# Optimization experiments

Measured on AMD Instinct MI355X. Metric: run time of the kernel, lower is better.

The kernel has to match this reference:

```python
import jax, jax.numpy as jnp
import numpy as np


def setup_inputs() -> dict:
    key = jax.random.key(0)
    k1, k2, k3 = jax.random.split(key, 3)
    N, D, C, G = 200000, 256, 512, 512
    x = jax.random.normal(k1, (N, D), dtype=jnp.float32)
    centroid_weight = jax.random.normal(k2, (C, D), dtype=jnp.float32)
    graph = jnp.sort(jax.random.randint(k3, (N,), 0, G, dtype=jnp.int64))
    return {"x": x, "centroid_weight": centroid_weight, "graph": graph, "num_graphs": G}


def reference(x, centroid_weight, graph, num_graphs):
    # EuclideanManifold: exp map at origin is the identity; dist is the L2 norm.
    # Pairwise node-to-centroid L2 distances via the GEMM identity
    # ||a-b||^2 = ||a||^2 + ||b||^2 - 2 a.b  (same math as the expanded
    # unsqueeze/expand path, without materializing the [N, C, D] tensor).
    x_sq = jnp.sum(x * x, axis=-1, keepdims=True)              # [N, 1]
    c_sq = jnp.sum(centroid_weight * centroid_weight, axis=-1)  # [C]
    sq = x_sq + c_sq[None, :] - 2.0 * jnp.einsum("nd,cd->nc", x, centroid_weight)
    dist = jnp.sqrt(jnp.maximum(sq, 0.0))                       # [N, C]

    # AvgPooling: per-graph mean of node-to-centroid distances.
    sums = jax.ops.segment_sum(dist, graph, num_segments=num_graphs)           # [G, C]
    counts = jax.ops.segment_sum(jnp.ones((dist.shape[0],), dist.dtype), graph,
                                 num_segments=num_graphs)                      # [G]
    return sums / jnp.maximum(counts, 1.0)[:, None]
```

## Files before the change

### kernel.cpp

```cpp
#include <hip/hip_runtime.h>
#include <hip/hip_bf16.h>

typedef __attribute__((ext_vector_type(8))) short short8;
typedef __attribute__((ext_vector_type(4))) float f32x4;
typedef __attribute__((ext_vector_type(2))) unsigned int uint2v;
typedef __attribute__((ext_vector_type(4))) unsigned int uint4v;

#define DK 256
#define BM 128
#define BN 128
#define BK 64
#define NKT 4

__device__ __forceinline__ unsigned int pack2bf(float lo, float hi) {
  return __builtin_amdgcn_perm(__builtin_bit_cast(unsigned int, hi),
                               __builtin_bit_cast(unsigned int, lo), 0x07060302);
}

__device__ __forceinline__ uint4v make_srsrc(const void* p, unsigned bytes) {
  union { const void* p; unsigned u[2]; } a; a.p = p;
  uint4v r;
  r.x = a.u[0];
  r.y = a.u[1] & 0xFFFFu;
  r.z = bytes;
  r.w = 0x00020000u;
  return r;
}

__global__ void __launch_bounds__(256)
prep_w(const float* __restrict__ w, unsigned short* __restrict__ wbf,
       float* __restrict__ csq) {
  const int b = blockIdx.x;
  const int ct = b >> 2, kt = b & 3;
  const int t = threadIdx.x;
  const int col = t >> 1, khalf = t & 1;
  const float* src = w + (size_t)(ct * BN + col) * DK + kt * BK + khalf * 32;
  unsigned char* dst = (unsigned char*)wbf + (size_t)b * 16384;
  const int sw = (col & 7) << 4;
  float s = 0.f;
  #pragma unroll
  for (int jc = 0; jc < 4; ++jc) {
    f32x4 v0 = *reinterpret_cast<const f32x4*>(src + jc * 8);
    f32x4 v1 = *reinterpret_cast<const f32x4*>(src + jc * 8 + 4);
    s += v0.x*v0.x + v0.y*v0.y + v0.z*v0.z + v0.w*v0.w
       + v1.x*v1.x + v1.y*v1.y + v1.z*v1.z + v1.w*v1.w;
    uint4v pk = { pack2bf(v0.x,v0.y), pack2bf(v0.z,v0.w),
                  pack2bf(v1.x,v1.y), pack2bf(v1.z,v1.w) };
    const int cidx = khalf * 4 + jc;
    *reinterpret_cast<uint4v*>(dst + ((col * 128 + cidx * 16) ^ sw)) = pk;
  }
  s += __shfl_xor(s, 1);
  if (khalf == 0) atomicAdd(&csq[ct * BN + col], s);
}

template<bool PREW>
__global__ void __launch_bounds__(256, 2)
centroid_gemm_pool(const float* __restrict__ x, const float* __restrict__ w,
                   const unsigned short* __restrict__ wbf,
                   const float* __restrict__ csqg, const int* __restrict__ graph,
                   float* __restrict__ outsum, int* __restrict__ cnt,
                   int N, int C, int row_tiles)
{
  __shared__ __align__(16) unsigned char lds_a[16384];
  __shared__ __align__(16) unsigned char lds_b[2][16384];
  __shared__ float xsq_lds[BM];
  __shared__ float csq_lds[BN];

  const int bid = blockIdx.x;
  const int xcd = bid & 7;
  const int j   = bid >> 3;
  const int ct  = j & 3;
  const int rt  = (j >> 2) * 8 + xcd;
  if (rt >= row_tiles) return;

  const int t    = threadIdx.x;
  const int lane = t & 63;
  const int wid  = t >> 6;
  const int wr   = wid >> 1, wc = wid & 1;
  const int h    = lane >> 4, l15 = lane & 15;

  const int g16 = t >> 4;
  const int sc4 = t & 15;
  const uint4v xrsrc = make_srsrc(x, (unsigned)((size_t)N * DK * 4));
  const unsigned voffA = (unsigned)(rt * BM + g16) * (DK * 4) + sc4 * 16;

  const int awbase = (g16 * 128 + sc4 * 8) ^ ((g16 & 7) << 4);
  const int base_a = (wr * 8192 + l15 * 128 + h * 16) ^ ((l15 & 7) << 4);
  const int base_b = (wc * 8192 + l15 * 128 + h * 16) ^ ((l15 & 7) << 4);

  const int rowg = rt * BM + wr * 64 + lane;
  int gl = (rowg < N) ? graph[rowg] : -1;
  asm volatile("" : "+v"(gl));

  f32x4 acc[4][4];
  #pragma unroll
  for (int mt = 0; mt < 4; ++mt)
    #pragma unroll
    for (int nt = 0; nt < 4; ++nt)
      acc[mt][nt] = (f32x4){0.f, 0.f, 0.f, 0.f};
  f32x4 accx[4];
  #pragma unroll
  for (int mt = 0; mt < 4; ++mt) accx[mt] = (f32x4){0.f, 0.f, 0.f, 0.f};
  float cq[8] = {0.f,0.f,0.f,0.f,0.f,0.f,0.f,0.f};

  f32x4 ra[8];
  auto loadA = [&](int kt) {
    #pragma unroll
    for (int q = 0; q < 8; ++q)
      asm volatile("buffer_load_dwordx4 %0, %1, %2, %3 offen"
                   : "=v"(ra[q])
                   : "v"(voffA), "s"(xrsrc), "s"(q * 16 * DK * 4 + kt * BK * 4));
  };
  auto cvtA = [&]() {
    #pragma unroll
    for (int q = 0; q < 8; ++q) {
      f32x4 v = ra[q];
      uint2v pk = { pack2bf(v.x, v.y), pack2bf(v.z, v.w) };
      *reinterpret_cast<uint2v*>(lds_a + awbase + q * 2048) = pk;
    }
  };
  auto stageB = [&](int buf, int kt) {
    const unsigned short* src = wbf + (((size_t)ct * 4 + kt) << 13) + t * 8;
    unsigned char* dst = lds_b[buf] + t * 16;
    #pragma unroll
    for (int p = 0; p < 4; ++p)
      __builtin_amdgcn_global_load_lds(src + p * 2048, dst + p * 4096, 16, 0, 0);
  };
  auto stageBsync = [&](int buf, int kt, bool accum) {
    #pragma unroll
    for (int q = 0; q < 8; ++q) {
      const int colq = q * 16 + g16;
      f32x4 v = *reinterpret_cast<const f32x4*>(
          w + (size_t)(ct * BN + colq) * DK + kt * BK + sc4 * 4);
      if (accum) cq[q] += v.x*v.x + v.y*v.y + v.z*v.z + v.w*v.w;
      uint2v pk = { pack2bf(v.x, v.y), pack2bf(v.z, v.w) };
      *reinterpret_cast<uint2v*>(lds_b[buf] + awbase + q * 2048) = pk;
    }
  };
  auto compute = [&](unsigned char* lb) {
    __builtin_amdgcn_s_setprio(1);
    #pragma unroll
    for (int kk = 0; kk < 2; ++kk) {
      short8 af[4], bfr[4];
      const int ka = base_a ^ (kk << 6);
      const int kb = base_b ^ (kk << 6);
      #pragma unroll
      for (int mt = 0; mt < 4; ++mt)
        af[mt] = *reinterpret_cast<const short8*>(lds_a + ka + mt * 2048);
      #pragma unroll
      for (int nt = 0; nt < 4; ++nt)
        bfr[nt] = *reinterpret_cast<const short8*>(lb + kb + nt * 2048);
      #pragma unroll
      for (int mt = 0; mt < 4; ++mt)
        #pragma unroll
        for (int nt = 0; nt < 4; ++nt)
          acc[mt][nt] = __builtin_amdgcn_mfma_f32_16x16x32_bf16(af[mt], bfr[nt], acc[mt][nt], 0, 0, 0);
      if (wc == 0) {
        #pragma unroll
        for (int mt = 0; mt < 4; ++mt)
          accx[mt] = __builtin_amdgcn_mfma_f32_16x16x32_bf16(af[mt], af[mt], accx[mt], 0, 0, 0);
      }
    }
    __builtin_amdgcn_s_setprio(0);
  };

  loadA(0);
  if (PREW) stageB(0, 0); else stageBsync(0, 0, true);

  #pragma unroll
  for (int kt = 0; kt < NKT; ++kt) {
    const int cur = kt & 1;
    if (PREW) { asm volatile("s_waitcnt vmcnt(4)" ::: "memory"); }
    else      { asm volatile("s_waitcnt vmcnt(0)" ::: "memory"); }
    __builtin_amdgcn_sched_barrier(0);
    cvtA();
    if (kt + 1 < NKT) {
      loadA(kt + 1);
      if (PREW) stageB(cur ^ 1, kt + 1);
      else      stageBsync(cur ^ 1, kt + 1, kt == 0);
      if (PREW) { asm volatile("s_waitcnt vmcnt(12)" ::: "memory"); }
      else      { asm volatile("s_waitcnt vmcnt(0)" ::: "memory"); }
    } else {
      asm volatile("s_waitcnt vmcnt(0)" ::: "memory");
    }
    asm volatile("s_waitcnt lgkmcnt(0)" ::: "memory");
    __builtin_amdgcn_sched_barrier(0);
    __builtin_amdgcn_s_barrier();
    __builtin_amdgcn_sched_barrier(0);
    compute(lds_b[cur]);
    __builtin_amdgcn_sched_barrier(0);
    __builtin_amdgcn_s_barrier();
    __builtin_amdgcn_sched_barrier(0);
  }

  if (wc == 0 && h == (l15 >> 2)) {
    #pragma unroll
    for (int mt = 0; mt < 4; ++mt)
      xsq_lds[wr * 64 + mt * 16 + l15] = accx[mt][l15 & 3];
  }
  if (!PREW) {
    #pragma unroll
    for (int q = 0; q < 8; ++q) {
      float sb = cq[q];
      sb += __shfl_xor(sb, 1); sb += __shfl_xor(sb, 2);
      sb += __shfl_xor(sb, 4); sb += __shfl_xor(sb, 8);
      if (l15 == 0) csq_lds[q * 16 + g16] = sb;
    }
  }
  __syncthreads();

  float xs[4][4], cs[4];
  #pragma unroll
  for (int mt = 0; mt < 4; ++mt)
    #pragma unroll
    for (int i = 0; i < 4; ++i)
      xs[mt][i] = xsq_lds[wr * 64 + mt * 16 + h * 4 + i];
  #pragma unroll
  for (int nt = 0; nt < 4; ++nt)
    cs[nt] = PREW ? csqg[ct * BN + wc * 64 + nt * 16 + l15]
                  : csq_lds[wc * 64 + nt * 16 + l15];
  #pragma unroll
  for (int mt = 0; mt < 4; ++mt)
    #pragma unroll
    for (int nt = 0; nt < 4; ++nt)
      #pragma unroll
      for (int i = 0; i < 4; ++i) {
        float dd = fmaf(-2.0f, acc[mt][nt][i], xs[mt][i] + cs[nt]);
        acc[mt][nt][i] = __builtin_amdgcn_sqrtf(fmaxf(dd, 0.f));
      }

  const int col0 = ct * BN + wc * 64;
  const int glp  = __shfl_up(gl, 1);
  const unsigned long long bmw = __ballot(lane == 0 || gl != glp);

  int s0 = 0;
  while (s0 < 64) {
    unsigned long long rest = (s0 < 63) ? (bmw >> (s0 + 1)) : 0ULL;
    const int e = rest ? s0 + 1 + __builtin_ctzll(rest) : 64;
    const int g = __shfl(gl, s0);
    if (g >= 0) {
      float p[4] = {0.f, 0.f, 0.f, 0.f};
      #pragma unroll
      for (int mt = 0; mt < 4; ++mt)
        #pragma unroll
        for (int i = 0; i < 4; ++i) {
          const int row = mt * 16 + h * 4 + i;
          const bool in = (row >= s0) && (row < e);
          #pragma unroll
          for (int nt = 0; nt < 4; ++nt)
            p[nt] += in ? acc[mt][nt][i] : 0.f;
        }
      #pragma unroll
      for (int nt = 0; nt < 4; ++nt) {
        p[nt] += __shfl_xor(p[nt], 16);
        p[nt] += __shfl_xor(p[nt], 32);
      }
      if (lane < 16) {
        #pragma unroll
        for (int nt = 0; nt < 4; ++nt)
          atomicAdd(&outsum[(size_t)g * C + col0 + nt * 16 + lane], p[nt]);
      }
      if (cnt && ct == 0 && wc == 0 && lane == 0)
        atomicAdd(&cnt[g], e - s0);
    }
    s0 = e;
  }
}

__global__ void __launch_bounds__(256)
divide_counts(float* __restrict__ out, const int* __restrict__ cnt, int C)
{
  const int g = blockIdx.x;
  const int c0 = cnt[g];
  const float inv = 1.0f / (float)(c0 > 1 ? c0 : 1);
  for (int c = threadIdx.x; c < C; c += 256)
    out[(size_t)g * C + c] *= inv;
}

__global__ void __launch_bounds__(128)
divide_by_count(float* __restrict__ out, const int* __restrict__ graph, int N, int C)
{
  const int g = blockIdx.x;
  int lo = 0, hi = N;
  while (lo < hi) { int mid = (lo + hi) >> 1; if (graph[mid] < g) lo = mid + 1; else hi = mid; }
  const int lb = lo;
  hi = N;
  while (lo < hi) { int mid = (lo + hi) >> 1; if (graph[mid] <= g) lo = mid + 1; else hi = mid; }
  const int cntg = lo - lb;
  const float inv = 1.0f / (float)(cntg > 1 ? cntg : 1);
  for (int c = threadIdx.x; c < C; c += blockDim.x)
    out[(size_t)g * C + c] *= inv;
}

extern "C" void kernel_launch(void* const* d_in, const int* in_sizes, int n_in,
                              void* d_out, int out_size, void* d_ws, size_t ws_size,
                              hipStream_t stream) {
  const float* x     = (const float*)d_in[0];
  const float* w     = (const float*)d_in[1];
  const int*   graph = (const int*)d_in[2];
  const int N = in_sizes[2];
  const int D = in_sizes[0] / N;
  const int C = in_sizes[1] / D;
  const int G = out_size / C;

  const int row_tiles = (N + BM - 1) / BM;
  const int rgroups   = (row_tiles + 7) / 8;
  const int grid      = rgroups * 8 * (C / BN);

  const size_t wbf_bytes = (size_t)16 * 16384;
  const size_t csq_off   = wbf_bytes;
  const size_t cnt_off   = wbf_bytes + (size_t)C * 4;
  const bool prew     = ws_size >= cnt_off + (size_t)G * 4;
  const bool have_cnt = prew || ws_size >= (size_t)G * 4;

  unsigned short* wbf = (unsigned short*)d_ws;
  float* csq = (float*)((char*)d_ws + csq_off);
  int*   cnt = prew ? (int*)((char*)d_ws + cnt_off)
                    : (have_cnt ? (int*)d_ws : nullptr);

  hipMemsetAsync(d_out, 0, (size_t)out_size * sizeof(float), stream);
  if (cnt) hipMemsetAsync(cnt, 0, (size_t)G * sizeof(int), stream);

  if (prew) {
    hipMemsetAsync(csq, 0, (size_t)C * sizeof(float), stream);
    prep_w<<<dim3(16), dim3(256), 0, stream>>>(w, wbf, csq);
    centroid_gemm_pool<true><<<dim3(grid), dim3(256), 0, stream>>>(
        x, w, wbf, csq, graph, (float*)d_out, cnt, N, C, row_tiles);
  } else {
    centroid_gemm_pool<false><<<dim3(grid), dim3(256), 0, stream>>>(
        x, w, wbf, csq, graph, (float*)d_out, cnt, N, C, row_tiles);
  }

  if (cnt)
    divide_counts<<<dim3(G), dim3(256), 0, stream>>>((float*)d_out, cnt, C);
  else
    divide_by_count<<<dim3(G), dim3(128), 0, stream>>>((float*)d_out, graph, N, C);
}
```

Before: 98.76 us.

## Give each wave private A rows and overlap B staging with compute

```diff
diff --git a/kernel.cpp b/kernel.cpp
--- a/kernel.cpp
+++ b/kernel.cpp
@@ -76,31 +76,31 @@
   const int t    = threadIdx.x;
   const int lane = t & 63;
   const int wid  = t >> 6;
-  const int wr   = wid >> 1, wc = wid & 1;
   const int h    = lane >> 4, l15 = lane & 15;
+
+  const uint4v xrsrc = make_srsrc(x, (unsigned)((size_t)N * DK * 4));
+  const unsigned voffA = (unsigned)(rt * BM + wid * 32 + h) * (DK * 4) + l15 * 16;
+
+  const int base_a = wid * 4096 + ((l15 * 128 + h * 16) ^ ((l15 & 7) << 4));
+  const int base_b = (l15 * 128 + h * 16) ^ ((l15 & 7) << 4);
 
   const int g16 = t >> 4;
   const int sc4 = t & 15;
-  const uint4v xrsrc = make_srsrc(x, (unsigned)((size_t)N * DK * 4));
-  const unsigned voffA = (unsigned)(rt * BM + g16) * (DK * 4) + sc4 * 16;
-
-  const int awbase = (g16 * 128 + sc4 * 8) ^ ((g16 & 7) << 4);
-  const int base_a = (wr * 8192 + l15 * 128 + h * 16) ^ ((l15 & 7) << 4);
-  const int base_b = (wc * 8192 + l15 * 128 + h * 16) ^ ((l15 & 7) << 4);
-
-  const int rowg = rt * BM + wr * 64 + lane;
+  const int awbase_b = (g16 * 128 + sc4 * 8) ^ ((g16 & 7) << 4);
+
+  const int rowg = rt * BM + wid * 32 + (lane & 31);
   int gl = (rowg < N) ? graph[rowg] : -1;
   asm volatile("" : "+v"(gl));
 
-  f32x4 acc[4][4];
-  #pragma unroll
-  for (int mt = 0; mt < 4; ++mt)
-    #pragma unroll
-    for (int nt = 0; nt < 4; ++nt)
+  f32x4 acc[2][8];
+  #pragma unroll
+  for (int mt = 0; mt < 2; ++mt)
+    #pragma unroll
+    for (int nt = 0; nt < 8; ++nt)
       acc[mt][nt] = (f32x4){0.f, 0.f, 0.f, 0.f};
-  f32x4 accx[4];
-  #pragma unroll
-  for (int mt = 0; mt < 4; ++mt) accx[mt] = (f32x4){0.f, 0.f, 0.f, 0.f};
+  f32x4 accx[2];
+  accx[0] = (f32x4){0.f,0.f,0.f,0.f};
+  accx[1] = (f32x4){0.f,0.f,0.f,0.f};
   float cq[8] = {0.f,0.f,0.f,0.f,0.f,0.f,0.f,0.f};
 
   f32x4 ra[8];
@@ -109,14 +109,16 @@
     for (int q = 0; q < 8; ++q)
       asm volatile("buffer_load_dwordx4 %0, %1, %2, %3 offen"
                    : "=v"(ra[q])
-                   : "v"(voffA), "s"(xrsrc), "s"(q * 16 * DK * 4 + kt * BK * 4));
+                   : "v"(voffA), "s"(xrsrc), "s"(q * 4096 + kt * 256));
   };
   auto cvtA = [&]() {
     #pragma unroll
     for (int q = 0; q < 8; ++q) {
       f32x4 v = ra[q];
       uint2v pk = { pack2bf(v.x, v.y), pack2bf(v.z, v.w) };
-      *reinterpret_cast<uint2v*>(lds_a + awbase + q * 2048) = pk;
+      const int rl = q * 4 + h;
+      *reinterpret_cast<uint2v*>(lds_a + wid * 4096 +
+          ((rl * 128 + l15 * 8) ^ ((rl & 7) << 4))) = pk;
     }
   };
   auto stageB = [&](int buf, int kt) {
@@ -134,32 +136,25 @@
           w + (size_t)(ct * BN + colq) * DK + kt * BK + sc4 * 4);
       if (accum) cq[q] += v.x*v.x + v.y*v.y + v.z*v.z + v.w*v.w;
       uint2v pk = { pack2bf(v.x, v.y), pack2bf(v.z, v.w) };
-      *reinterpret_cast<uint2v*>(lds_b[buf] + awbase + q * 2048) = pk;
+      *reinterpret_cast<uint2v*>(lds_b[buf] + awbase_b + q * 2048) = pk;
     }
   };
   auto compute = [&](unsigned char* lb) {
     __builtin_amdgcn_s_setprio(1);
     #pragma unroll
     for (int kk = 0; kk < 2; ++kk) {
-      short8 af[4], bfr[4];
       const int ka = base_a ^ (kk << 6);
       const int kb = base_b ^ (kk << 6);
+      short8 af0 = *reinterpret_cast<const short8*>(lds_a + ka);
+      short8 af1 = *reinterpret_cast<const short8*>(lds_a + ka + 2048);
       #pragma unroll
-      for (int mt = 0; mt < 4; ++mt)
-        af[mt] = *reinterpret_cast<const short8*>(lds_a + ka + mt * 2048);
-      #pragma unroll
-      for (int nt = 0; nt < 4; ++nt)
-        bfr[nt] = *reinterpret_cast<const short8*>(lb + kb + nt * 2048);
-      #pragma unroll
-      for (int mt = 0; mt < 4; ++mt)
-        #pragma unroll
-        for (int nt = 0; nt < 4; ++nt)
-          acc[mt][nt] = __builtin_amdgcn_mfma_f32_16x16x32_bf16(af[mt], bfr[nt], acc[mt][nt], 0, 0, 0);
-      if (wc == 0) {
-        #pragma unroll
-        for (int mt = 0; mt < 4; ++mt)
-          accx[mt] = __builtin_amdgcn_mfma_f32_16x16x32_bf16(af[mt], af[mt], accx[mt], 0, 0, 0);
+      for (int nt = 0; nt < 8; ++nt) {
+        short8 bfr = *reinterpret_cast<const short8*>(lb + kb + nt * 2048);
+        acc[0][nt] = __builtin_amdgcn_mfma_f32_16x16x32_bf16(af0, bfr, acc[0][nt], 0, 0, 0);
+        acc[1][nt] = __builtin_amdgcn_mfma_f32_16x16x32_bf16(af1, bfr, acc[1][nt], 0, 0, 0);
       }
+      accx[0] = __builtin_amdgcn_mfma_f32_16x16x32_bf16(af0, af0, accx[0], 0, 0, 0);
+      accx[1] = __builtin_amdgcn_mfma_f32_16x16x32_bf16(af1, af1, accx[1], 0, 0, 0);
     }
     __builtin_amdgcn_s_setprio(0);
   };
@@ -176,9 +171,7 @@
     cvtA();
     if (kt + 1 < NKT) {
       loadA(kt + 1);
-      if (PREW) stageB(cur ^ 1, kt + 1);
-      else      stageBsync(cur ^ 1, kt + 1, kt == 0);
-      if (PREW) { asm volatile("s_waitcnt vmcnt(12)" ::: "memory"); }
+      if (PREW) { asm volatile("s_waitcnt vmcnt(8)" ::: "memory"); }
       else      { asm volatile("s_waitcnt vmcnt(0)" ::: "memory"); }
     } else {
       asm volatile("s_waitcnt vmcnt(0)" ::: "memory");
@@ -187,16 +180,16 @@
     __builtin_amdgcn_sched_barrier(0);
     __builtin_amdgcn_s_barrier();
     __builtin_amdgcn_sched_barrier(0);
+    if (kt + 1 < NKT) {
+      if (PREW) stageB(cur ^ 1, kt + 1);
+      else      stageBsync(cur ^ 1, kt + 1, kt == 0);
+    }
     compute(lds_b[cur]);
-    __builtin_amdgcn_sched_barrier(0);
-    __builtin_amdgcn_s_barrier();
-    __builtin_amdgcn_sched_barrier(0);
-  }
-
-  if (wc == 0 && h == (l15 >> 2)) {
-    #pragma unroll
-    for (int mt = 0; mt < 4; ++mt)
-      xsq_lds[wr * 64 + mt * 16 + l15] = accx[mt][l15 & 3];
+  }
+
+  if (h == (l15 >> 2)) {
+    xsq_lds[wid * 32 + l15]      = accx[0][l15 & 3];
+    xsq_lds[wid * 32 + 16 + l15] = accx[1][l15 & 3];
   }
   if (!PREW) {
     #pragma unroll
@@ -206,61 +199,61 @@
       sb += __shfl_xor(sb, 4); sb += __shfl_xor(sb, 8);
       if (l15 == 0) csq_lds[q * 16 + g16] = sb;
     }
-  }
-  __syncthreads();
-
-  float xs[4][4], cs[4];
-  #pragma unroll
-  for (int mt = 0; mt < 4; ++mt)
+    __syncthreads();
+  }
+
+  float xs[2][4], cs[8];
+  #pragma unroll
+  for (int mt = 0; mt < 2; ++mt)
     #pragma unroll
     for (int i = 0; i < 4; ++i)
-      xs[mt][i] = xsq_lds[wr * 64 + mt * 16 + h * 4 + i];
-  #pragma unroll
-  for (int nt = 0; nt < 4; ++nt)
-    cs[nt] = PREW ? csqg[ct * BN + wc * 64 + nt * 16 + l15]
-                  : csq_lds[wc * 64 + nt * 16 + l15];
-  #pragma unroll
-  for (int mt = 0; mt < 4; ++mt)
-    #pragma unroll
-    for (int nt = 0; nt < 4; ++nt)
+      xs[mt][i] = xsq_lds[wid * 32 + mt * 16 + h * 4 + i];
+  #pragma unroll
+  for (int nt = 0; nt < 8; ++nt)
+    cs[nt] = PREW ? csqg[ct * BN + nt * 16 + l15] : csq_lds[nt * 16 + l15];
+  #pragma unroll
+  for (int mt = 0; mt < 2; ++mt)
+    #pragma unroll
+    for (int nt = 0; nt < 8; ++nt)
       #pragma unroll
       for (int i = 0; i < 4; ++i) {
         float dd = fmaf(-2.0f, acc[mt][nt][i], xs[mt][i] + cs[nt]);
         acc[mt][nt][i] = __builtin_amdgcn_sqrtf(fmaxf(dd, 0.f));
       }
 
-  const int col0 = ct * BN + wc * 64;
+  const int col0 = ct * BN;
   const int glp  = __shfl_up(gl, 1);
-  const unsigned long long bmw = __ballot(lane == 0 || gl != glp);
+  const unsigned int m32 =
+      (unsigned int)(__ballot(lane == 0 || gl != glp) & 0xffffffffull);
 
   int s0 = 0;
-  while (s0 < 64) {
-    unsigned long long rest = (s0 < 63) ? (bmw >> (s0 + 1)) : 0ULL;
-    const int e = rest ? s0 + 1 + __builtin_ctzll(rest) : 64;
+  while (s0 < 32) {
+    unsigned int rest = (s0 < 31) ? (m32 >> (s0 + 1)) : 0u;
+    const int e = rest ? s0 + 1 + __builtin_ctz(rest) : 32;
     const int g = __shfl(gl, s0);
     if (g >= 0) {
-      float p[4] = {0.f, 0.f, 0.f, 0.f};
+      float p[8] = {0.f,0.f,0.f,0.f,0.f,0.f,0.f,0.f};
       #pragma unroll
-      for (int mt = 0; mt < 4; ++mt)
+      for (int mt = 0; mt < 2; ++mt)
         #pragma unroll
         for (int i = 0; i < 4; ++i) {
           const int row = mt * 16 + h * 4 + i;
           const bool in = (row >= s0) && (row < e);
           #pragma unroll
-          for (int nt = 0; nt < 4; ++nt)
+          for (int nt = 0; nt < 8; ++nt)
             p[nt] += in ? acc[mt][nt][i] : 0.f;
         }
       #pragma unroll
-      for (int nt = 0; nt < 4; ++nt) {
+      for (int nt = 0; nt < 8; ++nt) {
         p[nt] += __shfl_xor(p[nt], 16);
         p[nt] += __shfl_xor(p[nt], 32);
       }
       if (lane < 16) {
         #pragma unroll
-        for (int nt = 0; nt < 4; ++nt)
+        for (int nt = 0; nt < 8; ++nt)
           atomicAdd(&outsum[(size_t)g * C + col0 + nt * 16 + lane], p[nt]);
       }
-      if (cnt && ct == 0 && wc == 0 && lane == 0)
+      if (cnt && ct == 0 && lane == 0)
         atomicAdd(&cnt[g], e - s0);
     }
     s0 = e;
```

New measurement: 104.0 us. +5.3%, slower.

## Process two row tiles per block with cross-tile load prefetch

Applied to the files above, without the earlier changes.

```diff
diff --git a/kernel.cpp b/kernel.cpp
--- a/kernel.cpp
+++ b/kernel.cpp
@@ -70,8 +70,11 @@
   const int xcd = bid & 7;
   const int j   = bid >> 3;
   const int ct  = j & 3;
-  const int rt  = (j >> 2) * 8 + xcd;
-  if (rt >= row_tiles) return;
+  const int rp  = (j >> 2) * 8 + xcd;
+  const int n_pairs = (row_tiles + 1) >> 1;
+  if (rp >= n_pairs) return;
+  const int rt0 = rp * 2;
+  const bool two = (rt0 + 1 < row_tiles);
 
   const int t    = threadIdx.x;
   const int lane = t & 63;
@@ -82,15 +85,20 @@
   const int g16 = t >> 4;
   const int sc4 = t & 15;
   const uint4v xrsrc = make_srsrc(x, (unsigned)((size_t)N * DK * 4));
-  const unsigned voffA = (unsigned)(rt * BM + g16) * (DK * 4) + sc4 * 16;
+  const unsigned voffA0 = (unsigned)(rt0 * BM + g16) * (DK * 4) + sc4 * 16;
 
   const int awbase = (g16 * 128 + sc4 * 8) ^ ((g16 & 7) << 4);
   const int base_a = (wr * 8192 + l15 * 128 + h * 16) ^ ((l15 & 7) << 4);
   const int base_b = (wc * 8192 + l15 * 128 + h * 16) ^ ((l15 & 7) << 4);
 
-  const int rowg = rt * BM + wr * 64 + lane;
-  int gl = (rowg < N) ? graph[rowg] : -1;
-  asm volatile("" : "+v"(gl));
+  int gl0, gl1;
+  {
+    const int r0 = rt0 * BM + wr * 64 + lane;
+    gl0 = (r0 < N) ? graph[r0] : -1;
+    const int r1 = r0 + BM;
+    gl1 = (two && r1 < N) ? graph[r1] : -1;
+  }
+  asm volatile("" : "+v"(gl0), "+v"(gl1));
 
   f32x4 acc[4][4];
   #pragma unroll
@@ -104,12 +112,12 @@
   float cq[8] = {0.f,0.f,0.f,0.f,0.f,0.f,0.f,0.f};
 
   f32x4 ra[8];
-  auto loadA = [&](int kt) {
+  auto loadA = [&](unsigned vo, int kt) {
     #pragma unroll
     for (int q = 0; q < 8; ++q)
       asm volatile("buffer_load_dwordx4 %0, %1, %2, %3 offen"
                    : "=v"(ra[q])
-                   : "v"(voffA), "s"(xrsrc), "s"(q * 16 * DK * 4 + kt * BK * 4));
+                   : "v"(vo), "s"(xrsrc), "s"(q * 16 * DK * 4 + kt * BK * 4));
   };
   auto cvtA = [&]() {
     #pragma unroll
@@ -164,106 +172,134 @@
     __builtin_amdgcn_s_setprio(0);
   };
 
-  loadA(0);
+  loadA(voffA0, 0);
   if (PREW) stageB(0, 0); else stageBsync(0, 0, true);
 
   #pragma unroll
-  for (int kt = 0; kt < NKT; ++kt) {
-    const int cur = kt & 1;
-    if (PREW) { asm volatile("s_waitcnt vmcnt(4)" ::: "memory"); }
-    else      { asm volatile("s_waitcnt vmcnt(0)" ::: "memory"); }
-    __builtin_amdgcn_sched_barrier(0);
-    cvtA();
-    if (kt + 1 < NKT) {
-      loadA(kt + 1);
-      if (PREW) stageB(cur ^ 1, kt + 1);
-      else      stageBsync(cur ^ 1, kt + 1, kt == 0);
-      if (PREW) { asm volatile("s_waitcnt vmcnt(12)" ::: "memory"); }
-      else      { asm volatile("s_waitcnt vmcnt(0)" ::: "memory"); }
-    } else {
-      asm volatile("s_waitcnt vmcnt(0)" ::: "memory");
-    }
-    asm volatile("s_waitcnt lgkmcnt(0)" ::: "memory");
-    __builtin_amdgcn_sched_barrier(0);
-    __builtin_amdgcn_s_barrier();
-    __builtin_amdgcn_sched_barrier(0);
-    compute(lds_b[cur]);
-    __builtin_amdgcn_sched_barrier(0);
-    __builtin_amdgcn_s_barrier();
-    __builtin_amdgcn_sched_barrier(0);
-  }
-
-  if (wc == 0 && h == (l15 >> 2)) {
+  for (int r2 = 0; r2 < 2; ++r2) {
+    if (r2 == 1 && !two) break;
+    const int rt = rt0 + r2;
+    const unsigned vo = voffA0 + (unsigned)r2 * (BM * DK * 4);
+    #pragma unroll
+    for (int kt = 0; kt < NKT; ++kt) {
+      const int cur = kt & 1;
+      if (PREW) {
+        if (r2 == 1 && kt == 0) { asm volatile("s_waitcnt vmcnt(0)" ::: "memory"); }
+        else                    { asm volatile("s_waitcnt vmcnt(4)" ::: "memory"); }
+      } else {
+        asm volatile("s_waitcnt vmcnt(0)" ::: "memory");
+      }
+      __builtin_amdgcn_sched_barrier(0);
+      cvtA();
+      const bool last_global = (kt == NKT - 1) && (r2 == 1 || !two);
+      if (!last_global) {
+        if (kt + 1 < NKT) {
+          loadA(vo, kt + 1);
+          if (PREW) stageB(cur ^ 1, kt + 1);
+          else      stageBsync(cur ^ 1, kt + 1, r2 == 0 && kt == 0);
+        } else {
+          loadA(vo + BM * DK * 4, 0);
+          if (PREW) stageB(cur ^ 1, 0);
+          else      stageBsync(cur ^ 1, 0, false);
+        }
+        if (PREW) { asm volatile("s_waitcnt vmcnt(12)" ::: "memory"); }
+        else      { asm volatile("s_waitcnt vmcnt(0)" ::: "memory"); }
+      } else {
+        asm volatile("s_waitcnt vmcnt(0)" ::: "memory");
+      }
+      asm volatile("s_waitcnt lgkmcnt(0)" ::: "memory");
+      __builtin_amdgcn_sched_barrier(0);
+      __builtin_amdgcn_s_barrier();
+      __builtin_amdgcn_sched_barrier(0);
+      compute(lds_b[cur]);
+      __builtin_amdgcn_sched_barrier(0);
+      __builtin_amdgcn_s_barrier();
+      __builtin_amdgcn_sched_barrier(0);
+    }
+
+    if (wc == 0 && h == (l15 >> 2)) {
+      #pragma unroll
+      for (int mt = 0; mt < 4; ++mt)
+        xsq_lds[wr * 64 + mt * 16 + l15] = accx[mt][l15 & 3];
+    }
+    if (!PREW && r2 == 0) {
+      #pragma unroll
+      for (int q = 0; q < 8; ++q) {
+        float sb = cq[q];
+        sb += __shfl_xor(sb, 1); sb += __shfl_xor(sb, 2);
+        sb += __shfl_xor(sb, 4); sb += __shfl_xor(sb, 8);
+        if (l15 == 0) csq_lds[q * 16 + g16] = sb;
+      }
+    }
+    __syncthreads();
+
+    float xs[4][4], cs[4];
     #pragma unroll
     for (int mt = 0; mt < 4; ++mt)
-      xsq_lds[wr * 64 + mt * 16 + l15] = accx[mt][l15 & 3];
-  }
-  if (!PREW) {
-    #pragma unroll
-    for (int q = 0; q < 8; ++q) {
-      float sb = cq[q];
-      sb += __shfl_xor(sb, 1); sb += __shfl_xor(sb, 2);
-      sb += __shfl_xor(sb, 4); sb += __shfl_xor(sb, 8);
-      if (l15 == 0) csq_lds[q * 16 + g16] = sb;
-    }
-  }
-  __syncthreads();
-
-  float xs[4][4], cs[4];
-  #pragma unroll
-  for (int mt = 0; mt < 4; ++mt)
-    #pragma unroll
-    for (int i = 0; i < 4; ++i)
-      xs[mt][i] = xsq_lds[wr * 64 + mt * 16 + h * 4 + i];
-  #pragma unroll
-  for (int nt = 0; nt < 4; ++nt)
-    cs[nt] = PREW ? csqg[ct * BN + wc * 64 + nt * 16 + l15]
-                  : csq_lds[wc * 64 + nt * 16 + l15];
-  #pragma unroll
-  for (int mt = 0; mt < 4; ++mt)
+      #pragma unroll
+      for (int i = 0; i < 4; ++i)
+        xs[mt][i] = xsq_lds[wr * 64 + mt * 16 + h * 4 + i];
     #pragma unroll
     for (int nt = 0; nt < 4; ++nt)
-      #pragma unroll
-      for (int i = 0; i < 4; ++i) {
-        float dd = fmaf(-2.0f, acc[mt][nt][i], xs[mt][i] + cs[nt]);
-        acc[mt][nt][i] = __builtin_amdgcn_sqrtf(fmaxf(dd, 0.f));
-      }
-
-  const int col0 = ct * BN + wc * 64;
-  const int glp  = __shfl_up(gl, 1);
-  const unsigned long long bmw = __ballot(lane == 0 || gl != glp);
-
-  int s0 = 0;
-  while (s0 < 64) {
-    unsigned long long rest = (s0 < 63) ? (bmw >> (s0 + 1)) : 0ULL;
-    const int e = rest ? s0 + 1 + __builtin_ctzll(rest) : 64;
-    const int g = __shfl(gl, s0);
-    if (g >= 0) {
-      float p[4] = {0.f, 0.f, 0.f, 0.f};
-      #pragma unroll
-      for (int mt = 0; mt < 4; ++mt)
+      cs[nt] = PREW ? csqg[ct * BN + wc * 64 + nt * 16 + l15]
+                    : csq_lds[wc * 64 + nt * 16 + l15];
+    #pragma unroll
+    for (int mt = 0; mt < 4; ++mt)
+      #pragma unroll
+      for (int nt = 0; nt < 4; ++nt)
         #pragma unroll
         for (int i = 0; i < 4; ++i) {
-          const int row = mt * 16 + h * 4 + i;
-          const bool in = (row >= s0) && (row < e);
+          float dd = fmaf(-2.0f, acc[mt][nt][i], xs[mt][i] + cs[nt]);
+          acc[mt][nt][i] = __builtin_amdgcn_sqrtf(fmaxf(dd, 0.f));
+        }
+
+    const int col0 = ct * BN + wc * 64;
+    const int gl   = r2 ? gl1 : gl0;
+    const int glp  = __shfl_up(gl, 1);
+    const unsigned long long bmw = __ballot(lane == 0 || gl != glp);
+
+    int s0 = 0;
+    while (s0 < 64) {
+      unsigned long long rest = (s0 < 63) ? (bmw >> (s0 + 1)) : 0ULL;
+      const int e = rest ? s0 + 1 + __builtin_ctzll(rest) : 64;
+      const int g = __shfl(gl, s0);
+      if (g >= 0) {
+        float p[4] = {0.f, 0.f, 0.f, 0.f};
+        #pragma unroll
+        for (int mt = 0; mt < 4; ++mt)
+          #pragma unroll
+          for (int i = 0; i < 4; ++i) {
+            const int row = mt * 16 + h * 4 + i;
+            const bool in = (row >= s0) && (row < e);
+            #pragma unroll
+            for (int nt = 0; nt < 4; ++nt)
+              p[nt] += in ? acc[mt][nt][i] : 0.f;
+          }
+        #pragma unroll
+        for (int nt = 0; nt < 4; ++nt) {
+          p[nt] += __shfl_xor(p[nt], 16);
+          p[nt] += __shfl_xor(p[nt], 32);
+        }
+        if (lane < 16) {
           #pragma unroll
           for (int nt = 0; nt < 4; ++nt)
-            p[nt] += in ? acc[mt][nt][i] : 0.f;
+            atomicAdd(&outsum[(size_t)g * C + col0 + nt * 16 + lane], p[nt]);
         }
-      #pragma unroll
-      for (int nt = 0; nt < 4; ++nt) {
-        p[nt] += __shfl_xor(p[nt], 16);
-        p[nt] += __shfl_xor(p[nt], 32);
-      }
-      if (lane < 16) {
+        if (cnt && ct == 0 && wc == 0 && lane == 0)
+          atomicAdd(&cnt[g], e - s0);
+      }
+      s0 = e;
+    }
+
+    if (r2 == 0 && two) {
+      #pragma unroll
+      for (int mt = 0; mt < 4; ++mt) {
         #pragma unroll
         for (int nt = 0; nt < 4; ++nt)
-          atomicAdd(&outsum[(size_t)g * C + col0 + nt * 16 + lane], p[nt]);
-      }
-      if (cnt && ct == 0 && wc == 0 && lane == 0)
-        atomicAdd(&cnt[g], e - s0);
-    }
-    s0 = e;
+          acc[mt][nt] = (f32x4){0.f, 0.f, 0.f, 0.f};
+        accx[mt] = (f32x4){0.f, 0.f, 0.f, 0.f};
+      }
+    }
   }
 }
 
@@ -304,8 +340,9 @@
   const int G = out_size / C;
 
   const int row_tiles = (N + BM - 1) / BM;
-  const int rgroups   = (row_tiles + 7) / 8;
-  const int grid      = rgroups * 8 * (C / BN);
+  const int n_pairs   = (row_tiles + 1) / 2;
+  const int pgroups   = (n_pairs + 7) / 8;
+  const int grid      = pgroups * 8 * (C / BN);
 
   const size_t wbf_bytes = (size_t)16 * 16384;
   const size_t csq_off   = wbf_bytes;
```

Result: slower. 112.6 us (+14.0%).
